# Kernel tuning notes

Hardware: AMD Instinct MI355X
Metric: run time of the kernel (lower is better)

Reference implementation:

```python
import jax, jax.numpy as jnp
import numpy as np

B, ORDER, N, D, H = 16, 2, 512, 128, 8
DH = D // H
NEG_SLOPE = 0.2


def setup_inputs() -> dict:
    key = jax.random.key(0)
    ks = jax.random.split(key, 8)
    stdv = 1.0 / np.sqrt(DH)

    def u(k, shape):
        return jax.random.uniform(k, shape, jnp.float32, -stdv, stdv)

    x = jax.random.normal(ks[0], (B, ORDER, N, D), jnp.float32)
    A = jax.random.randint(ks[1], (B, ORDER, N, N), 0, 5, jnp.int32)
    # Stacked params for the 2*order GAT modules: axis0 = order, axis1 = (conv1, conv2)
    W = u(ks[2], (ORDER, 2, D, D))            # project.weight
    pb = jnp.zeros((ORDER, 2, D), jnp.float32)  # project.bias (init 0)
    att_src = u(ks[3], (ORDER, 2, H, DH))
    att_dst = u(ks[4], (ORDER, 2, H, DH))
    bias = jnp.zeros((ORDER, 2, D), jnp.float32)  # GAT output bias (init 0)
    return {"x": x, "A": A, "W": W, "pb": pb,
            "att_src": att_src, "att_dst": att_dst, "bias": bias}


def _gat(x, Af, W, pb, a_src, a_dst, b):
    # x: [B,N,D]; Af: [B,N,N] float in {0,1}
    xp = x @ W.T + pb                                  # project
    xh = xp.reshape(B, N, H, DH)                       # [B,N,H,DH]
    s_src = jnp.einsum('bnhd,hd->bnh', xh, a_src)      # [B,N,H]
    s_dst = jnp.einsum('bnhd,hd->bnh', xh, a_dst)
    alpha = s_src[:, :, None, :] + s_dst[:, None, :, :]  # [B,src,dst,H]
    alpha = jnp.where((Af != 1.0)[..., None], 0.0, alpha)
    alpha = jnp.where(alpha >= 0, alpha, NEG_SLOPE * alpha)  # leaky relu
    alpha = jax.nn.softmax(alpha, axis=1)              # softmax over src dim
    out = jnp.einsum('bsdh,bshf->bdhf', alpha, xh).reshape(B, N, D)
    out = out + xp                                     # add_self_loops
    return out + b


def reference(x, A, W, pb, att_src, att_dst, bias):
    A1 = ((A == 2) | (A == 4)).astype(x.dtype)  # [B,ORDER,N,N]
    A2 = ((A == 3) | (A == 4)).astype(x.dtype)
    hs = []
    for i in range(ORDER):
        h1 = _gat(x[:, i], A1[:, i], W[i, 0], pb[i, 0], att_src[i, 0], att_dst[i, 0], bias[i, 0])
        h2 = _gat(x[:, i], A2[:, i], W[i, 1], pb[i, 1], att_src[i, 1], att_dst[i, 1], bias[i, 1])
        hs.append(h1 + h2)
    h = jnp.stack(hs, axis=1)                          # [B,ORDER,N,D]
    out = h + h.mean(axis=1, keepdims=True)
    return out
```

## Files before the change

### kernel.cpp

```cpp
#include <hip/hip_runtime.h>

#define N_ 512
#define D_ 128
#define LOG2E 1.44269504088896f


typedef __attribute__((ext_vector_type(8))) short short8;
typedef __attribute__((ext_vector_type(4))) float floatx4;
typedef __attribute__((ext_vector_type(4))) unsigned int uintx4;

#if defined(__has_builtin)
#if __has_builtin(__builtin_amdgcn_exp2f)
#define EXP2F(x) __builtin_amdgcn_exp2f(x)
#else
#define EXP2F(x) exp2f(x)
#endif
#else
#define EXP2F(x) exp2f(x)
#endif

__device__ __forceinline__ unsigned short f2bf(float f) {
    unsigned int u = __float_as_uint(f);
    u += 0x7fffu + ((u >> 16) & 1u);
    return (unsigned short)(u >> 16);
}
__device__ __forceinline__ float bflo(unsigned int u) { return __uint_as_float(u << 16); }
__device__ __forceinline__ float bfhi(unsigned int u) { return __uint_as_float(u & 0xffff0000u); }

__global__ __launch_bounds__(256) void proj_kernel(
    const float* __restrict__ x, const float* __restrict__ W,
    const float* __restrict__ pb, const float* __restrict__ att_src,
    const float* __restrict__ att_dst,
    unsigned short* __restrict__ xpt, float* __restrict__ sg)
{
    const int bid = blockIdx.x;
    const int unit = bid >> 1;
    const int half = bid & 1;
    const int ntile = unit & 7;
    const int inst  = unit >> 3;
    const int j = inst & 1;
    const int bi = inst >> 1;
    const int ij = (bi & 1) * 2 + j;
    const int t = threadIdx.x;
    const int wave = t >> 6, L = t & 63, n = L & 15, q = L >> 4;

    const int n0w = ntile * 64 + wave * 16;
    const float* xrow = x + ((size_t)bi * N_ + n0w + n) * D_ + q * 8;
    short8 Af[4];
#pragma unroll
    for (int kc = 0; kc < 4; ++kc) {
        const float4 a0 = *(const float4*)(xrow + kc * 32);
        const float4 a1 = *(const float4*)(xrow + kc * 32 + 4);
        uintx4 au;
        au.x = f2bf(a0.x) | ((unsigned int)f2bf(a0.y) << 16);
        au.y = f2bf(a0.z) | ((unsigned int)f2bf(a0.w) << 16);
        au.z = f2bf(a1.x) | ((unsigned int)f2bf(a1.y) << 16);
        au.w = f2bf(a1.z) | ((unsigned int)f2bf(a1.w) << 16);
        Af[kc] = __builtin_bit_cast(short8, au);
    }

    const float* wb = W + (size_t)ij * D_ * D_;
#pragma unroll
    for (int ft = 0; ft < 4; ++ft) {
        const int head = half * 4 + ft;
        const int fg = head * 16 + n;
        const float* wrow = wb + (size_t)fg * D_ + q * 8;
        floatx4 C = (floatx4){0.f, 0.f, 0.f, 0.f};
#pragma unroll
        for (int kc = 0; kc < 4; ++kc) {
            const float4 b0 = *(const float4*)(wrow + kc * 32);
            const float4 b1 = *(const float4*)(wrow + kc * 32 + 4);
            uintx4 bu;
            bu.x = f2bf(b0.x) | ((unsigned int)f2bf(b0.y) << 16);
            bu.y = f2bf(b0.z) | ((unsigned int)f2bf(b0.w) << 16);
            bu.z = f2bf(b1.x) | ((unsigned int)f2bf(b1.y) << 16);
            bu.w = f2bf(b1.z) | ((unsigned int)f2bf(b1.w) << 16);
            C = __builtin_amdgcn_mfma_f32_16x16x32_bf16(
                Af[kc], __builtin_bit_cast(short8, bu), C, 0, 0, 0);
        }
        const float pbv = pb[ij * D_ + fg];
        float xp0 = C[0] + pbv, xp1 = C[1] + pbv;
        float xp2 = C[2] + pbv, xp3 = C[3] + pbv;
        uint2 pk;
        pk.x = f2bf(xp0) | ((unsigned int)f2bf(xp1) << 16);
        pk.y = f2bf(xp2) | ((unsigned int)f2bf(xp3) << 16);
        *(uint2*)&xpt[((size_t)inst * D_ + fg) * N_ + n0w + q * 4] = pk;

        const float asv = att_src[ij * D_ + fg];
        const float adv = att_dst[ij * D_ + fg];
        float sa0 = xp0 * asv, sa1 = xp1 * asv, sa2 = xp2 * asv, sa3 = xp3 * asv;
        float sb0 = xp0 * adv, sb1 = xp1 * adv, sb2 = xp2 * adv, sb3 = xp3 * adv;
#pragma unroll
        for (int off = 1; off < 16; off <<= 1) {
            sa0 += __shfl_xor(sa0, off); sa1 += __shfl_xor(sa1, off);
            sa2 += __shfl_xor(sa2, off); sa3 += __shfl_xor(sa3, off);
            sb0 += __shfl_xor(sb0, off); sb1 += __shfl_xor(sb1, off);
            sb2 += __shfl_xor(sb2, off); sb3 += __shfl_xor(sb3, off);
        }
        if (n < 4) {
            const float v = (n == 0) ? sa0 : (n == 1) ? sa1 : (n == 2) ? sa2 : sa3;
            sg[(((size_t)inst * 2 + 0) * 8 + head) * N_ + n0w + q * 4 + n] = v * LOG2E;
        } else if (n >= 8 && n < 12) {
            const int r = n - 8;
            const float v = (r == 0) ? sb0 : (r == 1) ? sb1 : (r == 2) ? sb2 : sb3;
            sg[(((size_t)inst * 2 + 1) * 8 + head) * N_ + n0w + q * 4 + r] = v * LOG2E;
        }
    }
}

__global__ __launch_bounds__(256) void attn_kernel(
    const unsigned short* __restrict__ xpt,
    const float* __restrict__ sg,
    const int* __restrict__ A,
    const float* __restrict__ bias,
    float* __restrict__ hout)
{
    __shared__ float ss_t[2][8][N_];
    __shared__ unsigned int mask_l[2][N_];

    const int bid = blockIdx.x;
    const int tile = bid & 31;
    const int bi   = bid >> 5;
    const int i_ = bi & 1;
    const int d0 = tile * 16;
    const int t = threadIdx.x;
    const int wave = t >> 6, L = t & 63, n = L & 15, q = L >> 4;
    const int h0 = wave * 2;

#pragma unroll
    for (int rep = 0; rep < 2; ++rep) {
        const int s = t + rep * 256;
        const int* Ar = A + ((size_t)bi * N_ + s) * N_ + d0;
        unsigned int m0 = 0, m1 = 0;
#pragma unroll
        for (int g = 0; g < 4; ++g) {
            const int4 v = *(const int4*)(Ar + g * 4);
            const int k = g * 4;
            if (v.x == 2 || v.x == 4) m0 |= 1u << (k + 0);
            if (v.x == 3 || v.x == 4) m1 |= 1u << (k + 0);
            if (v.y == 2 || v.y == 4) m0 |= 1u << (k + 1);
            if (v.y == 3 || v.y == 4) m1 |= 1u << (k + 1);
            if (v.z == 2 || v.z == 4) m0 |= 1u << (k + 2);
            if (v.z == 3 || v.z == 4) m1 |= 1u << (k + 2);
            if (v.w == 2 || v.w == 4) m0 |= 1u << (k + 3);
            if (v.w == 3 || v.w == 4) m1 |= 1u << (k + 3);
        }
        mask_l[0][s] = m0;
        mask_l[1][s] = m1;
    }

#pragma unroll
    for (int j = 0; j < 2; ++j) {
        const float4* src = (const float4*)(sg + (size_t)((bi * 2 + j) * 2) * 8 * N_);
        float4* dst = (float4*)&ss_t[j][0][0];
#pragma unroll
        for (int r = 0; r < 4; ++r) dst[r * 256 + t] = src[r * 256 + t];
    }

    float sdv[2][2];
#pragma unroll
    for (int j = 0; j < 2; ++j)
#pragma unroll
        for (int hh = 0; hh < 2; ++hh)
            sdv[j][hh] = sg[(((size_t)(bi * 2 + j) * 2 + 1) * 8 + h0 + hh) * N_ + d0 + n];

    __syncthreads();

    const unsigned short* xpi[2] = { xpt + (size_t)(bi * 2) * D_ * N_,
                                     xpt + (size_t)(bi * 2 + 1) * D_ * N_ };

    const uintx4 ou = { 0x3F803F80u, 0x3F803F80u, 0x3F803F80u, 0x3F803F80u };
    const short8 onesB = __builtin_bit_cast(short8, ou);

    floatx4 Cacc[2][2], Cz[2][2];
#pragma unroll
    for (int j = 0; j < 2; ++j)
#pragma unroll
        for (int hh = 0; hh < 2; ++hh) {
            Cacc[j][hh] = (floatx4){0.f, 0.f, 0.f, 0.f};
            Cz[j][hh]   = (floatx4){0.f, 0.f, 0.f, 0.f};
        }

    for (int c = 0; c < 16; ++c) {
        const int sq = c * 32 + q * 8;
        short8 Bf[2][2];
#pragma unroll
        for (int j = 0; j < 2; ++j) {
            Bf[j][0] = *(const short8*)(xpi[j] + (size_t)(h0 * 16 + n) * N_ + sq);
            Bf[j][1] = *(const short8*)(xpi[j] + (size_t)((h0 + 1) * 16 + n) * N_ + sq);
        }
        const uint4 ma0 = *(const uint4*)&mask_l[0][sq];
        const uint4 ma1 = *(const uint4*)&mask_l[0][sq + 4];
        const uint4 mb0 = *(const uint4*)&mask_l[1][sq];
        const uint4 mb1 = *(const uint4*)&mask_l[1][sq + 4];
        const unsigned int mw[2][8] = {
            { ma0.x, ma0.y, ma0.z, ma0.w, ma1.x, ma1.y, ma1.z, ma1.w },
            { mb0.x, mb0.y, mb0.z, mb0.w, mb1.x, mb1.y, mb1.z, mb1.w } };
#pragma unroll
        for (int j = 0; j < 2; ++j) {
#pragma unroll
            for (int hh = 0; hh < 2; ++hh) {
                const float4 s0v = *(const float4*)&ss_t[j][h0 + hh][sq];
                const float4 s1v = *(const float4*)&ss_t[j][h0 + hh][sq + 4];
                const float ssv[8] = { s0v.x, s0v.y, s0v.z, s0v.w,
                                       s1v.x, s1v.y, s1v.z, s1v.w };
                unsigned int wt[8];
#pragma unroll
                for (int idx = 0; idx < 8; ++idx) {
                    const float z0 = ssv[idx] + sdv[j][hh];
                    const float zr = fmaxf(z0, 0.2f * z0);
                    const float e = EXP2F(zr);
                    wt[idx] = __float_as_uint(((mw[j][idx] >> n) & 1u) ? e : 1.0f);
                }
                uintx4 au;
                au.x = __builtin_amdgcn_perm(wt[1], wt[0], 0x07060302);
                au.y = __builtin_amdgcn_perm(wt[3], wt[2], 0x07060302);
                au.z = __builtin_amdgcn_perm(wt[5], wt[4], 0x07060302);
                au.w = __builtin_amdgcn_perm(wt[7], wt[6], 0x07060302);
                const short8 As = __builtin_bit_cast(short8, au);
                Cacc[j][hh] = __builtin_amdgcn_mfma_f32_16x16x32_bf16(
                    As, Bf[j][hh], Cacc[j][hh], 0, 0, 0);
                Cz[j][hh] = __builtin_amdgcn_mfma_f32_16x16x32_bf16(
                    As, onesB, Cz[j][hh], 0, 0, 0);
            }
        }
    }

    float hacc[2][4];
#pragma unroll
    for (int hh = 0; hh < 2; ++hh)
#pragma unroll
        for (int reg = 0; reg < 4; ++reg) hacc[hh][reg] = 0.f;

#pragma unroll
    for (int j = 0; j < 2; ++j) {
        const int ij = i_ * 2 + j;
#pragma unroll
        for (int hh = 0; hh < 2; ++hh) {
            const int h = h0 + hh;
            const float bv = bias[ij * D_ + h * 16 + n];
            const uint2 sv = *(const uint2*)(xpi[j] + (size_t)(h * 16 + n) * N_ + d0 + q * 4);
            const float selfv[4] = { bflo(sv.x), bfhi(sv.x), bflo(sv.y), bfhi(sv.y) };
#pragma unroll
            for (int reg = 0; reg < 4; ++reg) {
                const float Zi = 1.0f / Cz[j][hh][reg];
                hacc[hh][reg] += Cacc[j][hh][reg] * Zi + selfv[reg] + bv;
            }
        }
    }

#pragma unroll
    for (int hh = 0; hh < 2; ++hh)
#pragma unroll
        for (int reg = 0; reg < 4; ++reg)
            hout[((size_t)bi * N_ + d0 + q * 4 + reg) * D_ + (h0 + hh) * 16 + n]
                = hacc[hh][reg];
}

__global__ __launch_bounds__(256) void combine_kernel(float* __restrict__ h)
{
    const int idx = blockIdx.x * 256 + threadIdx.x;
    const int b = idx >> 14;
    const int r = idx & 16383;
    float4* p0 = (float4*)h + (size_t)b * 32768 + r;
    float4* p1 = p0 + 16384;
    const float4 a = *p0;
    const float4 o = *p1;
    float4 r0, r1;
    r0.x = 1.5f * a.x + 0.5f * o.x;  r1.x = 1.5f * o.x + 0.5f * a.x;
    r0.y = 1.5f * a.y + 0.5f * o.y;  r1.y = 1.5f * o.y + 0.5f * a.y;
    r0.z = 1.5f * a.z + 0.5f * o.z;  r1.z = 1.5f * o.z + 0.5f * a.z;
    r0.w = 1.5f * a.w + 0.5f * o.w;  r1.w = 1.5f * o.w + 0.5f * a.w;
    *p0 = r0;
    *p1 = r1;
}

extern "C" void kernel_launch(void* const* d_in, const int* in_sizes, int n_in,
                              void* d_out, int out_size, void* d_ws, size_t ws_size,
                              hipStream_t stream)
{
    const float* x   = (const float*)d_in[0];
    const int*   A   = (const int*)d_in[1];
    const float* W   = (const float*)d_in[2];
    const float* pb  = (const float*)d_in[3];
    const float* as_ = (const float*)d_in[4];
    const float* ad_ = (const float*)d_in[5];
    const float* bs  = (const float*)d_in[6];

    unsigned short* xpt = (unsigned short*)d_ws;
    float* sg = (float*)(xpt + (size_t)64 * D_ * N_);
    float* h = (float*)d_out;

    proj_kernel<<<1024, 256, 0, stream>>>(x, W, pb, as_, ad_, xpt, sg);
    attn_kernel<<<1024, 256, 0, stream>>>(xpt, sg, A, bs, h);
    combine_kernel<<<1024, 256, 0, stream>>>(h);
}
```

Baseline: 161.4 us.

## Split attention blocks by head half, one head per wave, doubling grid

The attention kernel now assigns each wave a single head instead of two, and splits the eight heads across two blocks per (batch, tile), doubling the grid to 2048 blocks. The per-block shared score buffer is halved and per-thread accumulators shrink, which lowers register and LDS use and can raise occupancy and parallelism. The trade-off is that each block rebuilds the adjacency bitmask from the global int32 A tensor, so A reads and mask computation are duplicated twice per tile.

```diff
diff --git a/kernel.cpp b/kernel.cpp
--- a/kernel.cpp
+++ b/kernel.cpp
@@ -115,17 +115,18 @@
     const float* __restrict__ bias,
     float* __restrict__ hout)
 {
-    __shared__ float ss_t[2][8][N_];
+    __shared__ float ss_t[2][4][N_];
     __shared__ unsigned int mask_l[2][N_];
 
     const int bid = blockIdx.x;
-    const int tile = bid & 31;
-    const int bi   = bid >> 5;
+    const int hhalf = bid & 1;
+    const int tile = (bid >> 1) & 31;
+    const int bi   = bid >> 6;
     const int i_ = bi & 1;
     const int d0 = tile * 16;
     const int t = threadIdx.x;
     const int wave = t >> 6, L = t & 63, n = L & 15, q = L >> 4;
-    const int h0 = wave * 2;
+    const int h = hhalf * 4 + wave;
 
 #pragma unroll
     for (int rep = 0; rep < 2; ++rep) {
@@ -151,18 +152,17 @@
 
 #pragma unroll
     for (int j = 0; j < 2; ++j) {
-        const float4* src = (const float4*)(sg + (size_t)((bi * 2 + j) * 2) * 8 * N_);
+        const float4* src = (const float4*)(sg
+            + ((size_t)(bi * 2 + j) * 2 * 8 + hhalf * 4) * N_);
         float4* dst = (float4*)&ss_t[j][0][0];
 #pragma unroll
-        for (int r = 0; r < 4; ++r) dst[r * 256 + t] = src[r * 256 + t];
-    }
-
-    float sdv[2][2];
+        for (int r = 0; r < 2; ++r) dst[r * 256 + t] = src[r * 256 + t];
+    }
+
+    float sdv[2];
 #pragma unroll
     for (int j = 0; j < 2; ++j)
-#pragma unroll
-        for (int hh = 0; hh < 2; ++hh)
-            sdv[j][hh] = sg[(((size_t)(bi * 2 + j) * 2 + 1) * 8 + h0 + hh) * N_ + d0 + n];
+        sdv[j] = sg[(((size_t)(bi * 2 + j) * 2 + 1) * 8 + h) * N_ + d0 + n];
 
     __syncthreads();
 
@@ -172,23 +172,18 @@
     const uintx4 ou = { 0x3F803F80u, 0x3F803F80u, 0x3F803F80u, 0x3F803F80u };
     const short8 onesB = __builtin_bit_cast(short8, ou);
 
-    floatx4 Cacc[2][2], Cz[2][2];
-#pragma unroll
-    for (int j = 0; j < 2; ++j)
-#pragma unroll
-        for (int hh = 0; hh < 2; ++hh) {
-            Cacc[j][hh] = (floatx4){0.f, 0.f, 0.f, 0.f};
-            Cz[j][hh]   = (floatx4){0.f, 0.f, 0.f, 0.f};
-        }
+    floatx4 Cacc[2], Cz[2];
+#pragma unroll
+    for (int j = 0; j < 2; ++j) {
+        Cacc[j] = (floatx4){0.f, 0.f, 0.f, 0.f};
+        Cz[j]   = (floatx4){0.f, 0.f, 0.f, 0.f};
+    }
 
     for (int c = 0; c < 16; ++c) {
         const int sq = c * 32 + q * 8;
-        short8 Bf[2][2];
-#pragma unroll
-        for (int j = 0; j < 2; ++j) {
-            Bf[j][0] = *(const short8*)(xpi[j] + (size_t)(h0 * 16 + n) * N_ + sq);
-            Bf[j][1] = *(const short8*)(xpi[j] + (size_t)((h0 + 1) * 16 + n) * N_ + sq);
-        }
+        short8 Bf[2];
+        Bf[0] = *(const short8*)(xpi[0] + (size_t)(h * 16 + n) * N_ + sq);
+        Bf[1] = *(const short8*)(xpi[1] + (size_t)(h * 16 + n) * N_ + sq);
         const uint4 ma0 = *(const uint4*)&mask_l[0][sq];
         const uint4 ma1 = *(const uint4*)&mask_l[0][sq + 4];
         const uint4 mb0 = *(const uint4*)&mask_l[1][sq];
@@ -198,63 +193,48 @@
             { mb0.x, mb0.y, mb0.z, mb0.w, mb1.x, mb1.y, mb1.z, mb1.w } };
 #pragma unroll
         for (int j = 0; j < 2; ++j) {
-#pragma unroll
-            for (int hh = 0; hh < 2; ++hh) {
-                const float4 s0v = *(const float4*)&ss_t[j][h0 + hh][sq];
-                const float4 s1v = *(const float4*)&ss_t[j][h0 + hh][sq + 4];
-                const float ssv[8] = { s0v.x, s0v.y, s0v.z, s0v.w,
-                                       s1v.x, s1v.y, s1v.z, s1v.w };
-                unsigned int wt[8];
-#pragma unroll
-                for (int idx = 0; idx < 8; ++idx) {
-                    const float z0 = ssv[idx] + sdv[j][hh];
-                    const float zr = fmaxf(z0, 0.2f * z0);
-                    const float e = EXP2F(zr);
-                    wt[idx] = __float_as_uint(((mw[j][idx] >> n) & 1u) ? e : 1.0f);
-                }
-                uintx4 au;
-                au.x = __builtin_amdgcn_perm(wt[1], wt[0], 0x07060302);
-                au.y = __builtin_amdgcn_perm(wt[3], wt[2], 0x07060302);
-                au.z = __builtin_amdgcn_perm(wt[5], wt[4], 0x07060302);
-                au.w = __builtin_amdgcn_perm(wt[7], wt[6], 0x07060302);
-                const short8 As = __builtin_bit_cast(short8, au);
-                Cacc[j][hh] = __builtin_amdgcn_mfma_f32_16x16x32_bf16(
-                    As, Bf[j][hh], Cacc[j][hh], 0, 0, 0);
-                Cz[j][hh] = __builtin_amdgcn_mfma_f32_16x16x32_bf16(
-                    As, onesB, Cz[j][hh], 0, 0, 0);
+            const float4 s0v = *(const float4*)&ss_t[j][wave][sq];
+            const float4 s1v = *(const float4*)&ss_t[j][wave][sq + 4];
+            const float ssv[8] = { s0v.x, s0v.y, s0v.z, s0v.w,
+                                   s1v.x, s1v.y, s1v.z, s1v.w };
+            unsigned int wt[8];
+#pragma unroll
+            for (int idx = 0; idx < 8; ++idx) {
+                const float z0 = ssv[idx] + sdv[j];
+                const float zr = fmaxf(z0, 0.2f * z0);
+                const float e = EXP2F(zr);
+                wt[idx] = __float_as_uint(((mw[j][idx] >> n) & 1u) ? e : 1.0f);
             }
-        }
-    }
-
-    float hacc[2][4];
-#pragma unroll
-    for (int hh = 0; hh < 2; ++hh)
-#pragma unroll
-        for (int reg = 0; reg < 4; ++reg) hacc[hh][reg] = 0.f;
-
+            uintx4 au;
+            au.x = __builtin_amdgcn_perm(wt[1], wt[0], 0x07060302);
+            au.y = __builtin_amdgcn_perm(wt[3], wt[2], 0x07060302);
+            au.z = __builtin_amdgcn_perm(wt[5], wt[4], 0x07060302);
+            au.w = __builtin_amdgcn_perm(wt[7], wt[6], 0x07060302);
+            const short8 As = __builtin_bit_cast(short8, au);
+            Cacc[j] = __builtin_amdgcn_mfma_f32_16x16x32_bf16(
+                As, Bf[j], Cacc[j], 0, 0, 0);
+            Cz[j] = __builtin_amdgcn_mfma_f32_16x16x32_bf16(
+                As, onesB, Cz[j], 0, 0, 0);
+        }
+    }
+
+    float hacc[4] = { 0.f, 0.f, 0.f, 0.f };
 #pragma unroll
     for (int j = 0; j < 2; ++j) {
         const int ij = i_ * 2 + j;
-#pragma unroll
-        for (int hh = 0; hh < 2; ++hh) {
-            const int h = h0 + hh;
-            const float bv = bias[ij * D_ + h * 16 + n];
-            const uint2 sv = *(const uint2*)(xpi[j] + (size_t)(h * 16 + n) * N_ + d0 + q * 4);
-            const float selfv[4] = { bflo(sv.x), bfhi(sv.x), bflo(sv.y), bfhi(sv.y) };
-#pragma unroll
-            for (int reg = 0; reg < 4; ++reg) {
-                const float Zi = 1.0f / Cz[j][hh][reg];
-                hacc[hh][reg] += Cacc[j][hh][reg] * Zi + selfv[reg] + bv;
-            }
-        }
-    }
-
-#pragma unroll
-    for (int hh = 0; hh < 2; ++hh)
-#pragma unroll
-        for (int reg = 0; reg < 4; ++reg)
-            hout[((size_t)bi * N_ + d0 + q * 4 + reg) * D_ + (h0 + hh) * 16 + n]
-                = hacc[hh][reg];
+        const float bv = bias[ij * D_ + h * 16 + n];
+        const uint2 sv = *(const uint2*)(xpi[j] + (size_t)(h * 16 + n) * N_ + d0 + q * 4);
+        const float selfv[4] = { bflo(sv.x), bfhi(sv.x), bflo(sv.y), bfhi(sv.y) };
+#pragma unroll
+        for (int reg = 0; reg < 4; ++reg) {
+            const float Zi = 1.0f / Cz[j][reg];
+            hacc[reg] += Cacc[j][reg] * Zi + selfv[reg] + bv;
+        }
+    }
+
+#pragma unroll
+    for (int reg = 0; reg < 4; ++reg)
+        hout[((size_t)bi * N_ + d0 + q * 4 + reg) * D_ + h * 16 + n] = hacc[reg];
 }
 
 __global__ __launch_bounds__(256) void combine_kernel(float* __restrict__ h)
@@ -292,6 +272,6 @@
     float* h = (float*)d_out;
 
     proj_kernel<<<1024, 256, 0, stream>>>(x, W, pb, as_, ad_, xpt, sg);
-    attn_kernel<<<1024, 256, 0, stream>>>(xpt, sg, A, bs, h);
+    attn_kernel<<<2048, 256, 0, stream>>>(xpt, sg, A, bs, h);
     combine_kernel<<<1024, 256, 0, stream>>>(h);
 }
```

Result: slower. 179.3 us (+11.0%).
